# Optimization experiments

Hardware: AMD Instinct MI355X
Metric: run time of the kernel (lower is better)

The kernel has to match this reference:

```python
import jax, jax.numpy as jnp
import numpy as np

N, D = 16384, 2048


def setup_inputs() -> dict:
    key = jax.random.key(0)
    k1, k2 = jax.random.split(key)
    x = jax.random.normal(k1, (N, D), dtype=jnp.float32)
    mask = jax.random.randint(k2, (N, D), 0, 2) > 0
    return {"x": x, "mask": mask}


def _masked_sparsemax(z, m):
    """Project each row of z onto the simplex restricted to positions where m is True.

    Fully batched equivalent of the TF per-row map_fn/cond/boolean_mask version.
    z: [..., D] float, m: [..., D] bool. Returns p with p>=0, sum over active = 1
    (all-zeros row if no active entries).
    """
    d = z.shape[-1]
    num_active = jnp.sum(m, axis=-1, keepdims=True)                 # [..., 1] int
    # Masked entries sort to the tail (-inf), so the first num_active sorted
    # entries are exactly the active values in descending order.
    z_neg = jnp.where(m, z, -jnp.inf)
    z_sorted = -jnp.sort(-z_neg, axis=-1)                           # descending
    k_int = jnp.arange(1, d + 1)
    k = k_int.astype(z.dtype)
    active_pos = k_int <= num_active                                # [..., D]
    # cumsum over active sorted entries only (zeros beyond num_active)
    csum = jnp.cumsum(jnp.where(active_pos, z_sorted, 0.0), axis=-1)
    # support condition: z_(k) - (csum_k - 1)/k > 0  <=>  k*z_(k) > csum_k - 1
    cond = (z_sorted * k > (csum - 1.0)) & active_pos
    rho = jnp.sum(cond, axis=-1, keepdims=True)                     # support size
    rho_idx = jnp.clip(rho - 1, 0, d - 1)
    csum_rho = jnp.take_along_axis(csum, rho_idx, axis=-1)
    theta = (csum_rho - 1.0) / jnp.maximum(rho, 1).astype(z.dtype)
    p_valid = jnp.maximum(z - theta, 0.0)
    # TF invalid_branch fallback: uniform over active entries (unreachable in
    # exact arithmetic since k=1 always satisfies cond, kept for faithfulness)
    p_uniform = 1.0 / jnp.maximum(num_active, 1).astype(z.dtype)
    p = jnp.where(rho > 0, p_valid, p_uniform)
    return jnp.where(m & (num_active > 0), p, 0.0)


def reference(x, mask):
    # axis = -1: project along the last axis (the TF layer transposes the
    # chosen axis to last; with axis=-1 that transpose is the identity).
    return _masked_sparsemax(x, mask)
```

## Files before the change

kernel.cpp:

```cpp
#include <hip/hip_runtime.h>
#include <math.h>


constexpr int D   = 2048;
constexpr int TPB = 256;
constexpr int EPT = D / TPB;

__global__ __launch_bounds__(TPB) void sparsemax_kernel(
    const float* __restrict__ x,
    const int*   __restrict__ mask,
    float*       __restrict__ out)
{
    const int    row  = blockIdx.x;
    const int    t    = threadIdx.x;
    const size_t base = (size_t)row * D + (size_t)t * EPT;

    float4 a  = ((const float4*)(x    + base))[0];
    float4 b  = ((const float4*)(x    + base))[1];
    int4   ma = ((const int4*)  (mask + base))[0];
    int4   mb = ((const int4*)  (mask + base))[1];

    float z[EPT];
    z[0] = ma.x ? a.x : -INFINITY;
    z[1] = ma.y ? a.y : -INFINITY;
    z[2] = ma.z ? a.z : -INFINITY;
    z[3] = ma.w ? a.w : -INFINITY;
    z[4] = mb.x ? b.x : -INFINITY;
    z[5] = mb.y ? b.y : -INFINITY;
    z[6] = mb.z ? b.z : -INFINITY;
    z[7] = mb.w ? b.w : -INFINITY;

    __shared__ float s_red[8];
    __shared__ float s_bc[2];

    float theta = -INFINITY;
    float prevC = -1.0f;

    for (int it = 0; it < 128; ++it) {
        float ps = 0.0f, pc = 0.0f;
        #pragma unroll
        for (int k = 0; k < EPT; ++k) {
            if (z[k] > theta) { ps += z[k]; pc += 1.0f; }
        }
        #pragma unroll
        for (int off = 32; off > 0; off >>= 1) {
            ps += __shfl_down(ps, off, 64);
            pc += __shfl_down(pc, off, 64);
        }
        const int wid = t >> 6;
        if ((t & 63) == 0) { s_red[wid] = ps; s_red[4 + wid] = pc; }
        __syncthreads();
        if (t == 0) {
            s_bc[0] = s_red[0] + s_red[1] + s_red[2] + s_red[3];
            s_bc[1] = s_red[4] + s_red[5] + s_red[6] + s_red[7];
        }
        __syncthreads();
        const float S = s_bc[0];
        const float C = s_bc[1];
        if (C == 0.0f) { theta = INFINITY; break; }
        if (C == prevC) break;
        theta = (S - 1.0f) / C;
        prevC = C;
    }

    float4 o0, o1;
    o0.x = fmaxf(z[0] - theta, 0.0f);
    o0.y = fmaxf(z[1] - theta, 0.0f);
    o0.z = fmaxf(z[2] - theta, 0.0f);
    o0.w = fmaxf(z[3] - theta, 0.0f);
    o1.x = fmaxf(z[4] - theta, 0.0f);
    o1.y = fmaxf(z[5] - theta, 0.0f);
    o1.z = fmaxf(z[6] - theta, 0.0f);
    o1.w = fmaxf(z[7] - theta, 0.0f);
    ((float4*)(out + base))[0] = o0;
    ((float4*)(out + base))[1] = o1;
}

extern "C" void kernel_launch(void* const* d_in, const int* in_sizes, int n_in,
                              void* d_out, int out_size, void* d_ws, size_t ws_size,
                              hipStream_t stream) {
    const float* x    = (const float*)d_in[0];
    const int*   mask = (const int*)  d_in[1];
    float*       out  = (float*)d_out;
    const int n_rows = in_sizes[0] / D;
    sparsemax_kernel<<<n_rows, TPB, 0, stream>>>(x, mask, out);
}
```

Baseline: 315.0 us.

## Map one wavefront per row to drop block-level barriers in sparsemax iteration

Each row is now handled by a single 64-lane wavefront holding 32 elements per lane, with four rows per block, instead of a 256-thread block per row. The per-iteration threshold reduction becomes a pure xor-shuffle butterfly, so every lane holds the total and the shared-memory stores and two __syncthreads per iteration go away. Loads are restructured into coalesced float4 chunks strided by 256 elements. The cost is more registers per thread and four times fewer threads working on each row's element-wise passes.

```diff
diff --git a/kernel.cpp b/kernel.cpp
--- a/kernel.cpp
+++ b/kernel.cpp
@@ -2,36 +2,36 @@
 #include <math.h>
 
 
-constexpr int D   = 2048;
-constexpr int TPB = 256;
-constexpr int EPT = D / TPB;
+constexpr int D    = 2048;
+constexpr int WPB  = 4;
+constexpr int TPB  = WPB * 64;
+constexpr int EPT  = D / 64;
+constexpr int CHK  = EPT / 4;
 
 __global__ __launch_bounds__(TPB) void sparsemax_kernel(
     const float* __restrict__ x,
     const int*   __restrict__ mask,
-    float*       __restrict__ out)
+    float*       __restrict__ out,
+    int n_rows)
 {
-    const int    row  = blockIdx.x;
-    const int    t    = threadIdx.x;
-    const size_t base = (size_t)row * D + (size_t)t * EPT;
+    const int wave = threadIdx.x >> 6;
+    const int lane = threadIdx.x & 63;
+    const int row  = blockIdx.x * WPB + wave;
+    if (row >= n_rows) return;
 
-    float4 a  = ((const float4*)(x    + base))[0];
-    float4 b  = ((const float4*)(x    + base))[1];
-    int4   ma = ((const int4*)  (mask + base))[0];
-    int4   mb = ((const int4*)  (mask + base))[1];
+    const size_t rbase = (size_t)row * D;
 
     float z[EPT];
-    z[0] = ma.x ? a.x : -INFINITY;
-    z[1] = ma.y ? a.y : -INFINITY;
-    z[2] = ma.z ? a.z : -INFINITY;
-    z[3] = ma.w ? a.w : -INFINITY;
-    z[4] = mb.x ? b.x : -INFINITY;
-    z[5] = mb.y ? b.y : -INFINITY;
-    z[6] = mb.z ? b.z : -INFINITY;
-    z[7] = mb.w ? b.w : -INFINITY;
-
-    __shared__ float s_red[8];
-    __shared__ float s_bc[2];
+    #pragma unroll
+    for (int c = 0; c < CHK; ++c) {
+        const size_t off = rbase + (size_t)(c * 256 + lane * 4);
+        const float4 a = *(const float4*)(x    + off);
+        const int4   m = *(const int4*)  (mask + off);
+        z[c * 4 + 0] = m.x ? a.x : -INFINITY;
+        z[c * 4 + 1] = m.y ? a.y : -INFINITY;
+        z[c * 4 + 2] = m.z ? a.z : -INFINITY;
+        z[c * 4 + 3] = m.w ? a.w : -INFINITY;
+    }
 
     float theta = -INFINITY;
     float prevC = -1.0f;
@@ -44,36 +44,25 @@
         }
         #pragma unroll
         for (int off = 32; off > 0; off >>= 1) {
-            ps += __shfl_down(ps, off, 64);
-            pc += __shfl_down(pc, off, 64);
+            ps += __shfl_xor(ps, off, 64);
+            pc += __shfl_xor(pc, off, 64);
         }
-        const int wid = t >> 6;
-        if ((t & 63) == 0) { s_red[wid] = ps; s_red[4 + wid] = pc; }
-        __syncthreads();
-        if (t == 0) {
-            s_bc[0] = s_red[0] + s_red[1] + s_red[2] + s_red[3];
-            s_bc[1] = s_red[4] + s_red[5] + s_red[6] + s_red[7];
-        }
-        __syncthreads();
-        const float S = s_bc[0];
-        const float C = s_bc[1];
-        if (C == 0.0f) { theta = INFINITY; break; }
-        if (C == prevC) break;
-        theta = (S - 1.0f) / C;
-        prevC = C;
+        if (pc == 0.0f) { theta = INFINITY; break; }
+        if (pc == prevC) break;
+        theta = (ps - 1.0f) / pc;
+        prevC = pc;
     }
 
-    float4 o0, o1;
-    o0.x = fmaxf(z[0] - theta, 0.0f);
-    o0.y = fmaxf(z[1] - theta, 0.0f);
-    o0.z = fmaxf(z[2] - theta, 0.0f);
-    o0.w = fmaxf(z[3] - theta, 0.0f);
-    o1.x = fmaxf(z[4] - theta, 0.0f);
-    o1.y = fmaxf(z[5] - theta, 0.0f);
-    o1.z = fmaxf(z[6] - theta, 0.0f);
-    o1.w = fmaxf(z[7] - theta, 0.0f);
-    ((float4*)(out + base))[0] = o0;
-    ((float4*)(out + base))[1] = o1;
+    #pragma unroll
+    for (int c = 0; c < CHK; ++c) {
+        const size_t off = rbase + (size_t)(c * 256 + lane * 4);
+        float4 o;
+        o.x = fmaxf(z[c * 4 + 0] - theta, 0.0f);
+        o.y = fmaxf(z[c * 4 + 1] - theta, 0.0f);
+        o.z = fmaxf(z[c * 4 + 2] - theta, 0.0f);
+        o.w = fmaxf(z[c * 4 + 3] - theta, 0.0f);
+        *(float4*)(out + off) = o;
+    }
 }
 
 extern "C" void kernel_launch(void* const* d_in, const int* in_sizes, int n_in,
@@ -83,5 +72,6 @@
     const int*   mask = (const int*)  d_in[1];
     float*       out  = (float*)d_out;
     const int n_rows = in_sizes[0] / D;
-    sparsemax_kernel<<<n_rows, TPB, 0, stream>>>(x, mask, out);
+    const int blocks = (n_rows + WPB - 1) / WPB;
+    sparsemax_kernel<<<blocks, TPB, 0, stream>>>(x, mask, out, n_rows);
 }
```

New measurement: 313.6 us. Within noise of the previous version (-0.4%).
